# Performance work log

Measured on AMD Instinct MI355X. Metric: run time of the kernel, lower is better.

## Reference

```python
import jax, jax.numpy as jnp
import numpy as np

B, T, C = 4, 2048, 1024
H = 16                      # n_head
D = C // H                  # head dim = 64
FF = 4 * C                  # 4096


def setup_inputs() -> dict:
    key = jax.random.key(0)
    ks = jax.random.split(key, 9)
    s = 0.02
    return {
        "x": jax.random.normal(ks[0], (B, T, C), dtype=jnp.float32),
        # LayerNorm params (elementwise affine, default torch init)
        "ln1_w": jnp.ones((C,), jnp.float32),
        "ln1_b": jnp.zeros((C,), jnp.float32),
        "ln2_w": jnp.ones((C,), jnp.float32),
        "ln2_b": jnp.zeros((C,), jnp.float32),
        # attention weights, torch Linear layout [out, in], bias=False
        "w_attn": jax.random.normal(ks[1], (3 * C, C), jnp.float32) * s,
        "w_proj": jax.random.normal(ks[2], (C, C), jnp.float32) * s,
        # FFN weights
        "w_fc": jax.random.normal(ks[3], (FF, C), jnp.float32) * s,
        "w_fc_proj": jax.random.normal(ks[4], (C, FF), jnp.float32) * s,
    }


def _layernorm(x, w, b, eps=1e-5):
    mu = jnp.mean(x, axis=-1, keepdims=True)
    var = jnp.var(x, axis=-1, keepdims=True)
    return (x - mu) * jax.lax.rsqrt(var + eps) * w + b


def _attn(h, w_attn, w_proj):
    qkv = jnp.einsum('btc,fc->btf', h, w_attn)        # [B,T,3C]
    q, k, v = jnp.split(qkv, 3, axis=-1)
    q = q.reshape(B, T, H, D).transpose(0, 2, 1, 3)   # [B,H,T,D]
    k = k.reshape(B, T, H, D).transpose(0, 2, 1, 3)
    v = v.reshape(B, T, H, D).transpose(0, 2, 1, 3)
    att = jnp.einsum('bhtd,bhsd->bhts', q, k) * (1.0 / np.sqrt(D))
    causal = jnp.tril(jnp.ones((T, T), dtype=bool))
    att = jnp.where(causal, att, -jnp.inf)
    att = jax.nn.softmax(att, axis=-1)
    y = jnp.einsum('bhts,bhsd->bhtd', att, v)         # [B,H,T,D]
    y = y.transpose(0, 2, 1, 3).reshape(B, T, C)
    return jnp.einsum('btc,oc->bto', y, w_proj)


def _ffn(h, w_fc, w_fc_proj):
    u = jax.nn.gelu(jnp.einsum('btc,fc->btf', h, w_fc), approximate=False)
    return jnp.einsum('btf,cf->btc', u, w_fc_proj)


def reference(x, ln1_w, ln1_b, ln2_w, ln2_b, w_attn, w_proj, w_fc, w_fc_proj):
    x = x + _attn(_layernorm(x, ln1_w, ln1_b), w_attn, w_proj)
    x = x + _ffn(_layernorm(x, ln2_w, ln2_b), w_fc, w_fc_proj)
    return x
```

## Files before the change

### kernel.cpp

```cpp
#include <hip/hip_runtime.h>
#include <hip/hip_bf16.h>

using bf16 = __hip_bfloat16;
typedef __attribute__((ext_vector_type(8))) short short8;
typedef __attribute__((ext_vector_type(4))) short sh4;
typedef __attribute__((ext_vector_type(4))) float f32x4;

#define B_ 4
#define T_ 2048
#define C_ 1024
#define H_ 16
#define FF_ 4096
#define M_TOK (B_ * T_)
#define SCALE2 0.1803368801111f

#define BARRIER() asm volatile("s_barrier" ::: "memory")
#define WAITLGKM0() asm volatile("s_waitcnt lgkmcnt(0)" ::: "memory")
#define WAITLGKM8() asm volatile("s_waitcnt lgkmcnt(8)" ::: "memory")
#define WAITVM4() asm volatile("s_waitcnt vmcnt(4)" ::: "memory")
#define WAITVM2() asm volatile("s_waitcnt vmcnt(2)" ::: "memory")
#define WAITVM0() asm volatile("s_waitcnt vmcnt(0)" ::: "memory")

__device__ __forceinline__ void gload16(const void* g, void* l) {
    __builtin_amdgcn_global_load_lds(
        (const __attribute__((address_space(1))) void*)g,
        (__attribute__((address_space(3))) void*)l, 16, 0, 0);
}

__device__ __forceinline__ float fexp2(float x) {
    float r;
    asm("v_exp_f32 %0, %1" : "=v"(r) : "v"(x));
    return r;
}

__device__ __forceinline__ float bf16bits2f(short s) {
    return __uint_as_float(((unsigned)(unsigned short)s) << 16);
}

__device__ __forceinline__ unsigned bf2(float a, float b) {
    bf16 x = __float2bfloat16(a), y = __float2bfloat16(b);
    unsigned short ux = *(unsigned short*)&x, uy = *(unsigned short*)&y;
    return (unsigned)ux | ((unsigned)uy << 16);
}

__device__ __forceinline__ float fgelu(float x) {
    float y = 0.79788456f * (x + 0.044715f * x * x * x);
    float tv = fexp2(y * 2.885390082f);
    return x * tv * __builtin_amdgcn_rcpf(tv + 1.f);
}

__global__ __launch_bounds__(256) void prep_kernel(
    const float* __restrict__ x, const float* __restrict__ ln1w, const float* __restrict__ ln1b,
    bf16* __restrict__ ln_out,
    const float* __restrict__ w_attn, const float* __restrict__ w_proj,
    const float* __restrict__ w_fc, const float* __restrict__ w_fcp,
    bf16* __restrict__ wattn_h, bf16* __restrict__ wproj_h,
    bf16* __restrict__ wfc_h, bf16* __restrict__ wfcp_h) {
    const int bid = blockIdx.x;
    const int t = threadIdx.x;
    if (bid < M_TOK) {
        float4 v = ((const float4*)(x + (size_t)bid * C_))[t];
        float s = v.x + v.y + v.z + v.w;
        float s2 = v.x * v.x + v.y * v.y + v.z * v.z + v.w * v.w;
#pragma unroll
        for (int off = 32; off > 0; off >>= 1) {
            s += __shfl_down(s, off);
            s2 += __shfl_down(s2, off);
        }
        __shared__ float ss[4], ss2[4];
        int wave = t >> 6, lane = t & 63;
        if (lane == 0) { ss[wave] = s; ss2[wave] = s2; }
        __syncthreads();
        s = ss[0] + ss[1] + ss[2] + ss[3];
        s2 = ss2[0] + ss2[1] + ss2[2] + ss2[3];
        float mu = s * (1.f / C_);
        float var = s2 * (1.f / C_) - mu * mu;
        float rstd = rsqrtf(var + 1e-5f);
        float4 wv = ((const float4*)ln1w)[t];
        float4 bv = ((const float4*)ln1b)[t];
        uint2 o;
        o.x = bf2((v.x - mu) * rstd * wv.x + bv.x, (v.y - mu) * rstd * wv.y + bv.y);
        o.y = bf2((v.z - mu) * rstd * wv.z + bv.z, (v.w - mu) * rstd * wv.w + bv.w);
        ((uint2*)(ln_out + (size_t)bid * C_))[t] = o;
    } else {
        int i = (bid - M_TOK) * 256 + t;
        const float* src;
        bf16* dst;
        int base;
        if (i < 786432) {
            src = w_attn; dst = wattn_h; base = 0;
        } else if (i < 1048576) {
            src = w_proj; dst = wproj_h; base = 786432;
        } else if (i < 2097152) {
            src = w_fc; dst = wfc_h; base = 1048576;
        } else {
            src = w_fcp; dst = wfcp_h; base = 2097152;
        }
        int j = i - base;
        float4 v = ((const float4*)src)[j];
        uint2 o;
        o.x = bf2(v.x, v.y);
        o.y = bf2(v.z, v.w);
        ((uint2*)dst)[j] = o;
    }
}

__global__ __launch_bounds__(256) void ln_kernel_b(const bf16* __restrict__ x,
                                                   const float* __restrict__ w,
                                                   const float* __restrict__ b,
                                                   bf16* __restrict__ out) {
    int row = blockIdx.x;
    int t = threadIdx.x;
    sh4 h = ((const sh4*)(x + (size_t)row * C_))[t];
    float4 v;
    v.x = bf16bits2f(h[0]);
    v.y = bf16bits2f(h[1]);
    v.z = bf16bits2f(h[2]);
    v.w = bf16bits2f(h[3]);
    float s = v.x + v.y + v.z + v.w;
    float s2 = v.x * v.x + v.y * v.y + v.z * v.z + v.w * v.w;
#pragma unroll
    for (int off = 32; off > 0; off >>= 1) {
        s += __shfl_down(s, off);
        s2 += __shfl_down(s2, off);
    }
    __shared__ float ss[4], ss2[4];
    int wave = t >> 6, lane = t & 63;
    if (lane == 0) { ss[wave] = s; ss2[wave] = s2; }
    __syncthreads();
    s = ss[0] + ss[1] + ss[2] + ss[3];
    s2 = ss2[0] + ss2[1] + ss2[2] + ss2[3];
    float mu = s * (1.f / C_);
    float var = s2 * (1.f / C_) - mu * mu;
    float rstd = rsqrtf(var + 1e-5f);
    float4 wv = ((const float4*)w)[t];
    float4 bv = ((const float4*)b)[t];
    uint2 o;
    o.x = bf2((v.x - mu) * rstd * wv.x + bv.x, (v.y - mu) * rstd * wv.y + bv.y);
    o.y = bf2((v.z - mu) * rstd * wv.z + bv.z, (v.w - mu) * rstd * wv.w + bv.w);
    ((uint2*)(out + (size_t)row * C_))[t] = o;
}

#define STG(ldsbase, g, grow0, k0)                                               \
    {                                                                            \
        _Pragma("unroll") for (int s_ = 0; s_ < 2; s_++) {                       \
            int row_ = s_ * 64 + wid * 8 + sr;                                   \
            gload16(g + (size_t)((grow0) + row_) * K + (k0) + ssc,               \
                    (ldsbase) + row_ * 64 + (lane & 7) * 8);                     \
        }                                                                        \
    }

#define HALF256 (128 * 64)
template <int EPI>
__global__ __launch_bounds__(512, 2) void gemm256(const bf16* __restrict__ Ag,
                                                  const bf16* __restrict__ Bg,
                                                  void* __restrict__ Cout,
                                                  int M, int N, int K) {
    __shared__ short SA[2][256 * 64];
    __shared__ short SB[2][256 * 64];

    const int nbx = N >> 8;
    const int nwg = nbx * (M >> 8);
    const int bid = blockIdx.x;
    const int cpx = nwg >> 3;
    const int swzb = (bid & 7) * cpx + (bid >> 3);
    const int m0 = (swzb / nbx) * 256;
    const int n0 = (swzb % nbx) * 256;

    const int t = threadIdx.x;
    const int wid = t >> 6, lane = t & 63;
    const int wm = wid >> 2, wn = wid & 3;
    const int lrow = lane & 15, lg = lane >> 4;
    const int swzr = (lane & 7) * 8;
    const int sr = lane >> 3;
    const int ssc = ((lane & 7) ^ sr) * 8;

    f32x4 acc[8][4];
#pragma unroll
    for (int mi = 0; mi < 8; mi++)
#pragma unroll
        for (int ni = 0; ni < 4; ni++) acc[mi][ni] = (f32x4){0.f, 0.f, 0.f, 0.f};
    short8 bfr[4][2];

    const int T = K >> 6;
    const int niter = T >> 1;

#define DSREADS256(q, buf)                                                       \
    if ((q) == 0) {                                                              \
        _Pragma("unroll") for (int ni = 0; ni < 4; ni++)                         \
        _Pragma("unroll") for (int ks = 0; ks < 2; ks++)                         \
            bfr[ni][ks] = *(const short8*)(&SB[buf][(wn * 64 + ni * 16 + lrow) * 64 + \
                                                    ((ks * 32 + lg * 8) ^ swzr)]);    \
    }                                                                            \
    _Pragma("unroll") for (int mi2 = 0; mi2 < 2; mi2++)                          \
    _Pragma("unroll") for (int ks = 0; ks < 2; ks++)                             \
        af[mi2 * 2 + ks] = *(const short8*)(&SA[buf][(wm * 128 + (2 * (q) + mi2) * 16 + lrow) * 64 + \
                                                     ((ks * 32 + lg * 8) ^ swzr)]);

#define MFMAS256(q)                                                              \
    __builtin_amdgcn_s_setprio(1);                                               \
    _Pragma("unroll") for (int ks = 0; ks < 2; ks++)                             \
    _Pragma("unroll") for (int ni = 0; ni < 4; ni++)                             \
    _Pragma("unroll") for (int mi2 = 0; mi2 < 2; mi2++)                          \
        acc[2 * (q) + mi2][ni] = __builtin_amdgcn_mfma_f32_16x16x32_bf16(        \
            bfr[ni][ks], af[mi2 * 2 + ks], acc[2 * (q) + mi2][ni], 0, 0, 0);     \
    __builtin_amdgcn_s_setprio(0);

    STG(&SA[0][0], Ag, m0, 0);
    STG(&SA[0][HALF256], Ag, m0 + 128, 0);
    STG(&SB[0][0], Bg, n0, 0);
    STG(&SB[0][HALF256], Bg, n0 + 128, 0);
    STG(&SB[1][0], Bg, n0, 64);
    STG(&SB[1][HALF256], Bg, n0 + 128, 64);
    WAITVM4();
    BARRIER();

    for (int iter = 0; iter < niter; iter++) {
        const int tt = 2 * iter;
        const int ka = (tt + 1) * 64, kb = (tt + 2) * 64, kc = (tt + 3) * 64;
        const bool s2 = (tt + 2 < T), s3 = (tt + 3 < T);
        const bool last = (iter == niter - 1);
        short8 af[4];

        DSREADS256(0, 0);
        STG(&SA[1][0], Ag, m0, ka);
        WAITLGKM8();
        BARRIER(); WAITLGKM0(); MFMAS256(0); BARRIER();
        DSREADS256(1, 0);
        STG(&SA[1][HALF256], Ag, m0 + 128, ka);
        BARRIER(); WAITLGKM0(); MFMAS256(1); BARRIER();
        DSREADS256(2, 0);
        if (s2) STG(&SB[0][0], Bg, n0, kb);
        BARRIER(); WAITLGKM0(); MFMAS256(2); BARRIER();
        DSREADS256(3, 0);
        if (s2) STG(&SB[0][HALF256], Bg, n0 + 128, kb);
        BARRIER(); WAITLGKM0(); MFMAS256(3);
        if (last) { WAITVM0(); } else { WAITVM4(); }
        BARRIER();
        DSREADS256(0, 1);
        if (s2) STG(&SA[0][0], Ag, m0, kb);
        WAITLGKM8();
        BARRIER(); WAITLGKM0(); MFMAS256(0); BARRIER();
        DSREADS256(1, 1);
        if (s2) STG(&SA[0][HALF256], Ag, m0 + 128, kb);
        BARRIER(); WAITLGKM0(); MFMAS256(1); BARRIER();
        DSREADS256(2, 1);
        if (s3) STG(&SB[1][0], Bg, n0, kc);
        BARRIER(); WAITLGKM0(); MFMAS256(2); BARRIER();
        DSREADS256(3, 1);
        if (s3) STG(&SB[1][HALF256], Bg, n0 + 128, kc);
        BARRIER(); WAITLGKM0(); MFMAS256(3);
        if (!last) WAITVM4();
        BARRIER();
    }

#pragma unroll
    for (int mi = 0; mi < 8; mi++) {
        const int gm = m0 + wm * 128 + mi * 16 + lrow;
#pragma unroll
        for (int ni = 0; ni < 4; ni++) {
            const int gn = n0 + wn * 64 + ni * 16 + lg * 4;
            size_t gi = (size_t)gm * N + gn;
            f32x4 a = acc[mi][ni];
            if constexpr (EPI == 0) {
                uint2 o; o.x = bf2(a[0], a[1]); o.y = bf2(a[2], a[3]);
                *(uint2*)&(((bf16*)Cout)[gi]) = o;
            } else if constexpr (EPI == 5) {
                float sc = (gn < C_) ? SCALE2 : 1.f;
                uint2 o; o.x = bf2(a[0] * sc, a[1] * sc); o.y = bf2(a[2] * sc, a[3] * sc);
                *(uint2*)&(((bf16*)Cout)[gi]) = o;
            } else {
                uint2 o;
                o.x = bf2(fgelu(a[0]), fgelu(a[1]));
                o.y = bf2(fgelu(a[2]), fgelu(a[3]));
                *(uint2*)&(((bf16*)Cout)[gi]) = o;
            }
        }
    }
}

template <int EPI>
__global__ __launch_bounds__(512, 2) void gemm256x128(const bf16* __restrict__ Ag,
                                                      const bf16* __restrict__ Bg,
                                                      void* __restrict__ Cout,
                                                      const void* __restrict__ Res,
                                                      int M, int N, int K) {
    __shared__ short SA[2][256 * 64];
    __shared__ short SB[2][128 * 64];

    const int nbx = N >> 7;
    const int nwg = nbx * (M >> 8);
    const int bid = blockIdx.x;
    const int cpx = nwg >> 3;
    const int swzb = (bid & 7) * cpx + (bid >> 3);
    const int m0 = (swzb / nbx) * 256;
    const int n0 = (swzb % nbx) * 128;

    const int t = threadIdx.x;
    const int wid = t >> 6, lane = t & 63;
    const int wm = wid >> 1, wn = wid & 1;
    const int lrow = lane & 15, lg = lane >> 4;
    const int swzr = (lane & 7) * 8;
    const int sr = lane >> 3;
    const int ssc = ((lane & 7) ^ sr) * 8;

    f32x4 acc[4][4];
#pragma unroll
    for (int mi = 0; mi < 4; mi++)
#pragma unroll
        for (int ni = 0; ni < 4; ni++) acc[mi][ni] = (f32x4){0.f, 0.f, 0.f, 0.f};
    short8 bfr[4][2];

    const int T = K >> 6;
    const int niter = T >> 1;

#define DSRX(p, buf)                                                             \
    if ((p) == 0) {                                                              \
        _Pragma("unroll") for (int ni = 0; ni < 4; ni++)                         \
        _Pragma("unroll") for (int ks = 0; ks < 2; ks++)                         \
            bfr[ni][ks] = *(const short8*)(&SB[buf][(wn * 64 + ni * 16 + lrow) * 64 + \
                                                    ((ks * 32 + lg * 8) ^ swzr)]);    \
    }                                                                            \
    _Pragma("unroll") for (int mi2 = 0; mi2 < 2; mi2++)                          \
    _Pragma("unroll") for (int ks = 0; ks < 2; ks++)                             \
        af[mi2 * 2 + ks] = *(const short8*)(&SA[buf][(wm * 64 + (2 * (p) + mi2) * 16 + lrow) * 64 + \
                                                     ((ks * 32 + lg * 8) ^ swzr)]);

#define MFX(p)                                                                   \
    __builtin_amdgcn_s_setprio(1);                                               \
    _Pragma("unroll") for (int ks = 0; ks < 2; ks++)                             \
    _Pragma("unroll") for (int ni = 0; ni < 4; ni++)                             \
    _Pragma("unroll") for (int mi2 = 0; mi2 < 2; mi2++)                          \
        acc[2 * (p) + mi2][ni] = __builtin_amdgcn_mfma_f32_16x16x32_bf16(        \
            bfr[ni][ks], af[mi2 * 2 + ks], acc[2 * (p) + mi2][ni], 0, 0, 0);     \
    __builtin_amdgcn_s_setprio(0);

    STG(&SA[0][0], Ag, m0, 0);
    STG(&SA[0][HALF256], Ag, m0 + 128, 0);
    STG(&SB[0][0], Bg, n0, 0);
    STG(&SB[1][0], Bg, n0, 64);
    WAITVM2();
    BARRIER();

    for (int iter = 0; iter < niter; iter++) {
        const int tt = 2 * iter;
        const int ka = (tt + 1) * 64, kb = (tt + 2) * 64, kc = (tt + 3) * 64;
        const bool s2 = (tt + 2 < T), s3 = (tt + 3 < T);
        const bool last = (iter == niter - 1);
        short8 af[4];

        DSRX(0, 0);
        STG(&SA[1][0], Ag, m0, ka);
        STG(&SA[1][HALF256], Ag, m0 + 128, ka);
        WAITLGKM8();
        BARRIER(); WAITLGKM0(); MFX(0); BARRIER();
        DSRX(1, 0);
        if (s2) STG(&SB[0][0], Bg, n0, kb);
        BARRIER(); WAITLGKM0(); MFX(1);
        if (last) { WAITVM0(); } else { WAITVM2(); }
        BARRIER();
        DSRX(0, 1);
        if (s2) {
            STG(&SA[0][0], Ag, m0, kb);
            STG(&SA[0][HALF256], Ag, m0 + 128, kb);
        }
        WAITLGKM8();
        BARRIER(); WAITLGKM0(); MFX(0); BARRIER();
        DSRX(1, 1);
        if (s3) STG(&SB[1][0], Bg, n0, kc);
        BARRIER(); WAITLGKM0(); MFX(1);
        if (last) { WAITVM0(); } else { WAITVM2(); }
        BARRIER();
    }

#pragma unroll
    for (int mi = 0; mi < 4; mi++) {
        const int gm = m0 + wm * 64 + mi * 16 + lrow;
#pragma unroll
        for (int ni = 0; ni < 4; ni++) {
            const int gn = n0 + wn * 64 + ni * 16 + lg * 4;
            size_t gi = (size_t)gm * N + gn;
            f32x4 a = acc[mi][ni];
            if constexpr (EPI == 0) {
                uint2 o; o.x = bf2(a[0], a[1]); o.y = bf2(a[2], a[3]);
                *(uint2*)&(((bf16*)Cout)[gi]) = o;
            } else if constexpr (EPI == 3) {
                float4 rv = *(const float4*)&(((const float*)Res)[gi]);
                uint2 o; o.x = bf2(rv.x + a[0], rv.y + a[1]); o.y = bf2(rv.z + a[2], rv.w + a[3]);
                *(uint2*)&(((bf16*)Cout)[gi]) = o;
            } else {
                sh4 hv = *(const sh4*)&(((const bf16*)Res)[gi]);
                float4 o;
                o.x = bf16bits2f(hv[0]) + a[0];
                o.y = bf16bits2f(hv[1]) + a[1];
                o.z = bf16bits2f(hv[2]) + a[2];
                o.w = bf16bits2f(hv[3]) + a[3];
                *(float4*)&(((float*)Cout)[gi]) = o;
            }
        }
    }
}

__global__ __launch_bounds__(256, 4) void flash_attn(const bf16* __restrict__ qk,
                                                     const bf16* __restrict__ vt,
                                                     bf16* __restrict__ y) {
    const int pi = blockIdx.x;
    const int bh = blockIdx.y;
    const int b = bh >> 4, h = bh & 15;
    const int t = threadIdx.x;
    const int wave = t >> 6, lane = t & 63;
    const int lrow = lane & 15, lg = lane >> 4, lk = lg * 8;

    __shared__ alignas(16) short Ks[64 * 72];
    __shared__ alignas(16) short Vs[64 * 72];
    __shared__ alignas(16) short Ps[64 * 72];

    const size_t rs = 2 * C_;
    const bf16* Qg = qk + (size_t)b * T_ * rs + h * 64;
    const bf16* Kg = Qg + C_;
    const bf16* Vg = vt + (size_t)(h * 64) * M_TOK + b * T_;

    const int srow = t >> 3;
    const int sc8 = (t & 7) * 8;

    for (int sel = 0; sel < 2; sel++) {
        const int qtb = sel ? pi : 31 - pi;
        const int q0 = qtb * 64;
        const int nkt = qtb + 1;
        const int qg = q0 + wave * 16 + lrow;

        short8 qf[2];
        {
            const bf16* qr = Qg + (size_t)qg * rs;
            qf[0] = *(const short8*)(qr + lk);
            qf[1] = *(const short8*)(qr + 32 + lk);
        }

        f32x4 o[4];
        float m1 = -1e30f, l1 = 0.f;
#pragma unroll
        for (int ni = 0; ni < 4; ni++) o[ni] = (f32x4){0.f, 0.f, 0.f, 0.f};

        short8 kr[2], vr[2];
#pragma unroll
        for (int p = 0; p < 2; p++) {
            int r = srow + p * 32;
            kr[p] = *(const short8*)(Kg + (size_t)r * rs + sc8);
            vr[p] = *(const short8*)(Vg + (size_t)r * M_TOK + sc8);
        }

        for (int kt = 0; kt < nkt; kt++) {
            const int s0 = kt * 64;
#pragma unroll
            for (int p = 0; p < 2; p++) {
                int r = srow + p * 32;
                *(short8*)(&Ks[r * 72 + sc8]) = kr[p];
                *(short8*)(&Vs[r * 72 + sc8]) = vr[p];
            }
            __syncthreads();
            if (kt + 1 < nkt) {
                const int s0n = (kt + 1) * 64;
#pragma unroll
                for (int p = 0; p < 2; p++) {
                    int r = srow + p * 32;
                    kr[p] = *(const short8*)(Kg + (size_t)(s0n + r) * rs + sc8);
                    vr[p] = *(const short8*)(Vg + (size_t)r * M_TOK + s0n + sc8);
                }
            }

            f32x4 s[4];
#pragma unroll
            for (int ni = 0; ni < 4; ni++) s[ni] = (f32x4){0.f, 0.f, 0.f, 0.f};
            __builtin_amdgcn_s_setprio(1);
#pragma unroll
            for (int ks = 0; ks < 2; ks++) {
#pragma unroll
                for (int ni = 0; ni < 4; ni++) {
                    short8 kf = *(const short8*)(&Ks[(ni * 16 + lrow) * 72 + ks * 32 + lk]);
                    s[ni] = __builtin_amdgcn_mfma_f32_16x16x32_bf16(kf, qf[ks], s[ni], 0, 0, 0);
                }
            }
            __builtin_amdgcn_s_setprio(0);

            if (kt == nkt - 1) {
#pragma unroll
                for (int ni = 0; ni < 4; ni++)
#pragma unroll
                    for (int r = 0; r < 4; r++) {
                        int kvg = s0 + ni * 16 + lg * 4 + r;
                        if (kvg > qg) s[ni][r] = -1e30f;
                    }
            }

            float pm = s[0][0];
#pragma unroll
            for (int ni = 0; ni < 4; ni++)
#pragma unroll
                for (int r = 0; r < 4; r++) pm = fmaxf(pm, s[ni][r]);
            pm = fmaxf(pm, __shfl_xor(pm, 16));
            pm = fmaxf(pm, __shfl_xor(pm, 32));
            if (!__all(pm - m1 <= 8.f)) {
                float mn = fmaxf(m1, pm);
                float alpha = fexp2(m1 - mn);
                m1 = mn;
                l1 *= alpha;
#pragma unroll
                for (int ni = 0; ni < 4; ni++)
#pragma unroll
                    for (int r = 0; r < 4; r++) o[ni][r] *= alpha;
            }
            float rsum = 0.f;
#pragma unroll
            for (int ni = 0; ni < 4; ni++) {
                float p0 = fexp2(s[ni][0] - m1);
                float p1 = fexp2(s[ni][1] - m1);
                float p2 = fexp2(s[ni][2] - m1);
                float p3 = fexp2(s[ni][3] - m1);
                rsum += (p0 + p1) + (p2 + p3);
                uint2 pk; pk.x = bf2(p0, p1); pk.y = bf2(p2, p3);
                *(uint2*)(&Ps[(wave * 16 + lrow) * 72 + ni * 16 + lg * 4]) = pk;
            }
            rsum += __shfl_xor(rsum, 16);
            rsum += __shfl_xor(rsum, 32);
            l1 += rsum;

            __builtin_amdgcn_s_setprio(1);
#pragma unroll
            for (int ks2 = 0; ks2 < 2; ks2++) {
                short8 pf = *(const short8*)(&Ps[(wave * 16 + lrow) * 72 + ks2 * 32 + lk]);
#pragma unroll
                for (int ni = 0; ni < 4; ni++) {
                    short8 vf = *(const short8*)(&Vs[(ni * 16 + lrow) * 72 + ks2 * 32 + lk]);
                    o[ni] = __builtin_amdgcn_mfma_f32_16x16x32_bf16(vf, pf, o[ni], 0, 0, 0);
                }
            }
            __builtin_amdgcn_s_setprio(0);
            __syncthreads();
        }

        float inv = 1.f / l1;
#pragma unroll
        for (int ni = 0; ni < 4; ni++) {
            uint2 pk;
            pk.x = bf2(o[ni][0] * inv, o[ni][1] * inv);
            pk.y = bf2(o[ni][2] * inv, o[ni][3] * inv);
            *(uint2*)(&y[((size_t)(b * T_ + qg)) * C_ + h * 64 + ni * 16 + lg * 4]) = pk;
        }
    }
}

extern "C" void kernel_launch(void* const* d_in, const int* in_sizes, int n_in,
                              void* d_out, int out_size, void* d_ws, size_t ws_size,
                              hipStream_t stream) {
    const float* x      = (const float*)d_in[0];
    const float* ln1w   = (const float*)d_in[1];
    const float* ln1b   = (const float*)d_in[2];
    const float* ln2w   = (const float*)d_in[3];
    const float* ln2b   = (const float*)d_in[4];
    const float* w_attn = (const float*)d_in[5];
    const float* w_proj = (const float*)d_in[6];
    const float* w_fc   = (const float*)d_in[7];
    const float* w_fcp  = (const float*)d_in[8];
    float* out = (float*)d_out;

    char* ws = (char*)d_ws;
    bf16* ln_buf  = (bf16*)(ws);
    bf16* qk_buf  = (bf16*)(ws + (16u << 20));
    bf16* vt_buf  = (bf16*)(ws + (48u << 20));
    bf16* ybuf    = (bf16*)(ws + (64u << 20));
    bf16* ubuf    = (bf16*)(ws + (16u << 20));
    bf16* x2b     = (bf16*)(ws + (80u << 20));
    bf16* wattn_h = (bf16*)(ws + (112u << 20));
    bf16* wproj_h = (bf16*)(ws + (118u << 20));
    bf16* wfc_h   = (bf16*)(ws + (120u << 20));
    bf16* wfcp_h  = (bf16*)(ws + (128u << 20));

    prep_kernel<<<M_TOK + 12288, 256, 0, stream>>>(
        x, ln1w, ln1b, ln_buf,
        w_attn, w_proj, w_fc, w_fcp,
        wattn_h, wproj_h, wfc_h, wfcp_h);

    gemm256<5><<<dim3((M_TOK / 256) * (2 * C_ / 256)), 512, 0, stream>>>(
        ln_buf, wattn_h, qk_buf, M_TOK, 2 * C_, C_);

    gemm256x128<0><<<dim3((C_ / 256) * (M_TOK / 128)), 512, 0, stream>>>(
        wattn_h + (size_t)2 * C_ * C_, ln_buf, vt_buf, nullptr, C_, M_TOK, C_);

    flash_attn<<<dim3(16, B_ * H_), 256, 0, stream>>>(qk_buf, vt_buf, ybuf);

    gemm256x128<3><<<dim3((M_TOK / 256) * (C_ / 128)), 512, 0, stream>>>(
        ybuf, wproj_h, x2b, x, M_TOK, C_, C_);

    ln_kernel_b<<<M_TOK, 256, 0, stream>>>(x2b, ln2w, ln2b, ln_buf);

    gemm256<2><<<dim3((M_TOK / 256) * (FF_ / 256)), 512, 0, stream>>>(
        ln_buf, wfc_h, ubuf, M_TOK, FF_, C_);

    gemm256x128<4><<<dim3((M_TOK / 256) * (C_ / 128)), 512, 0, stream>>>(
        ubuf, wfcp_h, out, x2b, M_TOK, C_, FF_);
}
```

Measured before the change: 354.9 us.

## Share K/V tile loads between paired causal query tiles in flash attention

Each block used to process its high and low query tiles one after the other, loading K/V tiles separately for each. Now both tiles are handled in a single KV loop, so each K/V tile staged in LDS serves both query tiles while kt <= ql. This roughly halves K/V global loads and LDS staging for the low tile, at the cost of more live registers (two sets of accumulators and Q fragments), which may hurt occupancy. The grid is also reordered so that blocks of different heads with the same pair index launch together.

Result: no change. 349.5 us (-1.5%).

```diff
diff --git a/kernel.cpp b/kernel.cpp
--- a/kernel.cpp
+++ b/kernel.cpp
@@ -404,8 +404,8 @@
 __global__ __launch_bounds__(256, 4) void flash_attn(const bf16* __restrict__ qk,
                                                      const bf16* __restrict__ vt,
                                                      bf16* __restrict__ y) {
-    const int pi = blockIdx.x;
-    const int bh = blockIdx.y;
+    const int bh = blockIdx.x;
+    const int pi = blockIdx.y;
     const int b = bh >> 4, h = bh & 15;
     const int t = threadIdx.x;
     const int wave = t >> 6, lane = t & 63;
@@ -423,72 +423,77 @@
     const int srow = t >> 3;
     const int sc8 = (t & 7) * 8;
 
-    for (int sel = 0; sel < 2; sel++) {
-        const int qtb = sel ? pi : 31 - pi;
-        const int q0 = qtb * 64;
-        const int nkt = qtb + 1;
-        const int qg = q0 + wave * 16 + lrow;
-
-        short8 qf[2];
-        {
-            const bf16* qr = Qg + (size_t)qg * rs;
-            qf[0] = *(const short8*)(qr + lk);
-            qf[1] = *(const short8*)(qr + 32 + lk);
-        }
-
-        f32x4 o[4];
-        float m1 = -1e30f, l1 = 0.f;
-#pragma unroll
-        for (int ni = 0; ni < 4; ni++) o[ni] = (f32x4){0.f, 0.f, 0.f, 0.f};
-
-        short8 kr[2], vr[2];
+    const int ql = pi, qh = 31 - pi;
+    const int nkt = qh + 1;
+    const int qgH = qh * 64 + wave * 16 + lrow;
+    const int qgL = ql * 64 + wave * 16 + lrow;
+
+    short8 qfH[2], qfL[2];
+    {
+        const bf16* qr = Qg + (size_t)qgH * rs;
+        qfH[0] = *(const short8*)(qr + lk);
+        qfH[1] = *(const short8*)(qr + 32 + lk);
+        qr = Qg + (size_t)qgL * rs;
+        qfL[0] = *(const short8*)(qr + lk);
+        qfL[1] = *(const short8*)(qr + 32 + lk);
+    }
+
+    f32x4 oH[4], oL[4];
+    float mH = -1e30f, lH = 0.f, mL = -1e30f, lL = 0.f;
+#pragma unroll
+    for (int ni = 0; ni < 4; ni++) {
+        oH[ni] = (f32x4){0.f, 0.f, 0.f, 0.f};
+        oL[ni] = (f32x4){0.f, 0.f, 0.f, 0.f};
+    }
+
+    short8 kr[2], vr[2];
+#pragma unroll
+    for (int p = 0; p < 2; p++) {
+        int r = srow + p * 32;
+        kr[p] = *(const short8*)(Kg + (size_t)r * rs + sc8);
+        vr[p] = *(const short8*)(Vg + (size_t)r * M_TOK + sc8);
+    }
+
+    for (int kt = 0; kt < nkt; kt++) {
+        const int s0 = kt * 64;
 #pragma unroll
         for (int p = 0; p < 2; p++) {
             int r = srow + p * 32;
-            kr[p] = *(const short8*)(Kg + (size_t)r * rs + sc8);
-            vr[p] = *(const short8*)(Vg + (size_t)r * M_TOK + sc8);
-        }
-
-        for (int kt = 0; kt < nkt; kt++) {
-            const int s0 = kt * 64;
+            *(short8*)(&Ks[r * 72 + sc8]) = kr[p];
+            *(short8*)(&Vs[r * 72 + sc8]) = vr[p];
+        }
+        __syncthreads();
+        if (kt + 1 < nkt) {
+            const int s0n = (kt + 1) * 64;
 #pragma unroll
             for (int p = 0; p < 2; p++) {
                 int r = srow + p * 32;
-                *(short8*)(&Ks[r * 72 + sc8]) = kr[p];
-                *(short8*)(&Vs[r * 72 + sc8]) = vr[p];
-            }
-            __syncthreads();
-            if (kt + 1 < nkt) {
-                const int s0n = (kt + 1) * 64;
-#pragma unroll
-                for (int p = 0; p < 2; p++) {
-                    int r = srow + p * 32;
-                    kr[p] = *(const short8*)(Kg + (size_t)(s0n + r) * rs + sc8);
-                    vr[p] = *(const short8*)(Vg + (size_t)r * M_TOK + s0n + sc8);
-                }
-            }
-
+                kr[p] = *(const short8*)(Kg + (size_t)(s0n + r) * rs + sc8);
+                vr[p] = *(const short8*)(Vg + (size_t)r * M_TOK + s0n + sc8);
+            }
+        }
+
+        {
             f32x4 s[4];
 #pragma unroll
             for (int ni = 0; ni < 4; ni++) s[ni] = (f32x4){0.f, 0.f, 0.f, 0.f};
             __builtin_amdgcn_s_setprio(1);
 #pragma unroll
-            for (int ks = 0; ks < 2; ks++) {
+            for (int ks = 0; ks < 2; ks++)
 #pragma unroll
                 for (int ni = 0; ni < 4; ni++) {
                     short8 kf = *(const short8*)(&Ks[(ni * 16 + lrow) * 72 + ks * 32 + lk]);
-                    s[ni] = __builtin_amdgcn_mfma_f32_16x16x32_bf16(kf, qf[ks], s[ni], 0, 0, 0);
+                    s[ni] = __builtin_amdgcn_mfma_f32_16x16x32_bf16(kf, qfH[ks], s[ni], 0, 0, 0);
                 }
-            }
             __builtin_amdgcn_s_setprio(0);
 
-            if (kt == nkt - 1) {
+            if (kt == qh) {
 #pragma unroll
                 for (int ni = 0; ni < 4; ni++)
 #pragma unroll
                     for (int r = 0; r < 4; r++) {
                         int kvg = s0 + ni * 16 + lg * 4 + r;
-                        if (kvg > qg) s[ni][r] = -1e30f;
+                        if (kvg > qgH) s[ni][r] = -1e30f;
                     }
             }
 
@@ -499,30 +504,30 @@
                 for (int r = 0; r < 4; r++) pm = fmaxf(pm, s[ni][r]);
             pm = fmaxf(pm, __shfl_xor(pm, 16));
             pm = fmaxf(pm, __shfl_xor(pm, 32));
-            if (!__all(pm - m1 <= 8.f)) {
-                float mn = fmaxf(m1, pm);
-                float alpha = fexp2(m1 - mn);
-                m1 = mn;
-                l1 *= alpha;
+            if (!__all(pm - mH <= 8.f)) {
+                float mn = fmaxf(mH, pm);
+                float alpha = fexp2(mH - mn);
+                mH = mn;
+                lH *= alpha;
 #pragma unroll
                 for (int ni = 0; ni < 4; ni++)
 #pragma unroll
-                    for (int r = 0; r < 4; r++) o[ni][r] *= alpha;
+                    for (int r = 0; r < 4; r++) oH[ni][r] *= alpha;
             }
             float rsum = 0.f;
 #pragma unroll
             for (int ni = 0; ni < 4; ni++) {
-                float p0 = fexp2(s[ni][0] - m1);
-                float p1 = fexp2(s[ni][1] - m1);
-                float p2 = fexp2(s[ni][2] - m1);
-                float p3 = fexp2(s[ni][3] - m1);
+                float p0 = fexp2(s[ni][0] - mH);
+                float p1 = fexp2(s[ni][1] - mH);
+                float p2 = fexp2(s[ni][2] - mH);
+                float p3 = fexp2(s[ni][3] - mH);
                 rsum += (p0 + p1) + (p2 + p3);
                 uint2 pk; pk.x = bf2(p0, p1); pk.y = bf2(p2, p3);
                 *(uint2*)(&Ps[(wave * 16 + lrow) * 72 + ni * 16 + lg * 4]) = pk;
             }
             rsum += __shfl_xor(rsum, 16);
             rsum += __shfl_xor(rsum, 32);
-            l1 += rsum;
+            lH += rsum;
 
             __builtin_amdgcn_s_setprio(1);
 #pragma unroll
@@ -531,21 +536,93 @@
 #pragma unroll
                 for (int ni = 0; ni < 4; ni++) {
                     short8 vf = *(const short8*)(&Vs[(ni * 16 + lrow) * 72 + ks2 * 32 + lk]);
-                    o[ni] = __builtin_amdgcn_mfma_f32_16x16x32_bf16(vf, pf, o[ni], 0, 0, 0);
+                    oH[ni] = __builtin_amdgcn_mfma_f32_16x16x32_bf16(vf, pf, oH[ni], 0, 0, 0);
                 }
             }
             __builtin_amdgcn_s_setprio(0);
-            __syncthreads();
-        }
-
-        float inv = 1.f / l1;
-#pragma unroll
-        for (int ni = 0; ni < 4; ni++) {
-            uint2 pk;
-            pk.x = bf2(o[ni][0] * inv, o[ni][1] * inv);
-            pk.y = bf2(o[ni][2] * inv, o[ni][3] * inv);
-            *(uint2*)(&y[((size_t)(b * T_ + qg)) * C_ + h * 64 + ni * 16 + lg * 4]) = pk;
-        }
+        }
+
+        if (kt <= ql) {
+            f32x4 s[4];
+#pragma unroll
+            for (int ni = 0; ni < 4; ni++) s[ni] = (f32x4){0.f, 0.f, 0.f, 0.f};
+            __builtin_amdgcn_s_setprio(1);
+#pragma unroll
+            for (int ks = 0; ks < 2; ks++)
+#pragma unroll
+                for (int ni = 0; ni < 4; ni++) {
+                    short8 kf = *(const short8*)(&Ks[(ni * 16 + lrow) * 72 + ks * 32 + lk]);
+                    s[ni] = __builtin_amdgcn_mfma_f32_16x16x32_bf16(kf, qfL[ks], s[ni], 0, 0, 0);
+                }
+            __builtin_amdgcn_s_setprio(0);
+
+            if (kt == ql) {
+#pragma unroll
+                for (int ni = 0; ni < 4; ni++)
+#pragma unroll
+                    for (int r = 0; r < 4; r++) {
+                        int kvg = s0 + ni * 16 + lg * 4 + r;
+                        if (kvg > qgL) s[ni][r] = -1e30f;
+                    }
+            }
+
+            float pm = s[0][0];
+#pragma unroll
+            for (int ni = 0; ni < 4; ni++)
+#pragma unroll
+                for (int r = 0; r < 4; r++) pm = fmaxf(pm, s[ni][r]);
+            pm = fmaxf(pm, __shfl_xor(pm, 16));
+            pm = fmaxf(pm, __shfl_xor(pm, 32));
+            if (!__all(pm - mL <= 8.f)) {
+                float mn = fmaxf(mL, pm);
+                float alpha = fexp2(mL - mn);
+                mL = mn;
+                lL *= alpha;
+#pragma unroll
+                for (int ni = 0; ni < 4; ni++)
+#pragma unroll
+                    for (int r = 0; r < 4; r++) oL[ni][r] *= alpha;
+            }
+            float rsum = 0.f;
+#pragma unroll
+            for (int ni = 0; ni < 4; ni++) {
+                float p0 = fexp2(s[ni][0] - mL);
+                float p1 = fexp2(s[ni][1] - mL);
+                float p2 = fexp2(s[ni][2] - mL);
+                float p3 = fexp2(s[ni][3] - mL);
+                rsum += (p0 + p1) + (p2 + p3);
+                uint2 pk; pk.x = bf2(p0, p1); pk.y = bf2(p2, p3);
+                *(uint2*)(&Ps[(wave * 16 + lrow) * 72 + ni * 16 + lg * 4]) = pk;
+            }
+            rsum += __shfl_xor(rsum, 16);
+            rsum += __shfl_xor(rsum, 32);
+            lL += rsum;
+
+            __builtin_amdgcn_s_setprio(1);
+#pragma unroll
+            for (int ks2 = 0; ks2 < 2; ks2++) {
+                short8 pf = *(const short8*)(&Ps[(wave * 16 + lrow) * 72 + ks2 * 32 + lk]);
+#pragma unroll
+                for (int ni = 0; ni < 4; ni++) {
+                    short8 vf = *(const short8*)(&Vs[(ni * 16 + lrow) * 72 + ks2 * 32 + lk]);
+                    oL[ni] = __builtin_amdgcn_mfma_f32_16x16x32_bf16(vf, pf, oL[ni], 0, 0, 0);
+                }
+            }
+            __builtin_amdgcn_s_setprio(0);
+        }
+        __syncthreads();
+    }
+
+    float invH = 1.f / lH, invL = 1.f / lL;
+#pragma unroll
+    for (int ni = 0; ni < 4; ni++) {
+        uint2 pk;
+        pk.x = bf2(oH[ni][0] * invH, oH[ni][1] * invH);
+        pk.y = bf2(oH[ni][2] * invH, oH[ni][3] * invH);
+        *(uint2*)(&y[((size_t)(b * T_ + qgH)) * C_ + h * 64 + ni * 16 + lg * 4]) = pk;
+        pk.x = bf2(oL[ni][0] * invL, oL[ni][1] * invL);
+        pk.y = bf2(oL[ni][2] * invL, oL[ni][3] * invL);
+        *(uint2*)(&y[((size_t)(b * T_ + qgL)) * C_ + h * 64 + ni * 16 + lg * 4]) = pk;
     }
 }
 
@@ -586,7 +663,7 @@
     gemm256x128<0><<<dim3((C_ / 256) * (M_TOK / 128)), 512, 0, stream>>>(
         wattn_h + (size_t)2 * C_ * C_, ln_buf, vt_buf, nullptr, C_, M_TOK, C_);
 
-    flash_attn<<<dim3(16, B_ * H_), 256, 0, stream>>>(qk_buf, vt_buf, ybuf);
+    flash_attn<<<dim3(B_ * H_, 16), 256, 0, stream>>>(qk_buf, vt_buf, ybuf);
 
     gemm256x128<3><<<dim3((M_TOK / 256) * (C_ / 128)), 512, 0, stream>>>(
         ybuf, wproj_h, x2b, x, M_TOK, C_, C_);
```
